# Optimization experiments

Measured on AMD Instinct MI355X. Metric: run time of the kernel, lower is better.

The kernel has to match this reference:

```python
import jax, jax.numpy as jnp
import numpy as np

TOPK = 2


def _conv2d(x, w, b):
    # x: (B, Cin, H, W), w: (Cout, Cin, 3, 3), SAME padding (padding=1)
    y = jax.lax.conv_general_dilated(
        x, w, window_strides=(1, 1), padding='SAME',
        dimension_numbers=('NCHW', 'OIHW', 'NCHW'))
    return y + b[None, :, None, None]


def _msunit(x2d, c1w, c1b, c2w, c2b):
    # TimesNet-style 2D unit: conv(1->d_model) -> GELU -> conv(d_model->1)
    h = jax.nn.gelu(_conv2d(x2d, c1w, c1b))
    return _conv2d(h, c2w, c2b)


def setup_inputs():
    B, T, H, DM = 256, 2048, 720, 64
    key = jax.random.key(0)
    ks = jax.random.split(key, 5)
    x = jax.random.normal(ks[0], (B, 1, T), jnp.float32)
    conv1_w = jax.random.normal(ks[1], (DM, 1, 3, 3), jnp.float32) * 0.1
    conv1_b = jnp.zeros((DM,), jnp.float32)
    conv2_w = jax.random.normal(ks[2], (1, DM, 3, 3), jnp.float32) * 0.1
    conv2_b = jnp.zeros((1,), jnp.float32)
    head_w = jax.random.normal(ks[3], (H, T), jnp.float32) * 0.02
    head_b = jnp.zeros((H,), jnp.float32)
    return {'x': x, 'conv1_w': conv1_w, 'conv1_b': conv1_b,
            'conv2_w': conv2_w, 'conv2_b': conv2_b,
            'head_w': head_w, 'head_b': head_b}


def reference(x, conv1_w, conv1_b, conv2_w, conv2_b, head_w, head_b):
    B, _, T = x.shape
    # FFT amplitude spectrum, batch-averaged, drop DC bin
    amp = jnp.abs(jnp.fft.rfft(x[:, 0, :], axis=-1)).mean(0)[1:]
    vals, idx = jax.lax.top_k(amp, TOPK)
    # data-dependent period selection (mirrors .item() calls in torch -> Python ints)
    freqs = np.asarray(idx) + 1
    P_list = [max(1, int(round(T / int(f)))) for f in freqs]
    weights = jax.nn.softmax(vals.astype(x.dtype))
    y = jnp.zeros_like(x)
    for i, P in enumerate(P_list):
        cols = (T + P - 1) // P
        pad = P * cols - T
        xp = jnp.pad(x, ((0, 0), (0, 0), (0, pad)))
        x2d = xp.reshape(B, 1, cols, P).transpose(0, 1, 3, 2)  # (B,1,P,cols)
        y2d = _msunit(x2d, conv1_w, conv1_b, conv2_w, conv2_b)  # (B,1,P,cols)
        y1d = y2d.transpose(0, 1, 3, 2).reshape(B, 1, cols * P)[..., :T]
        y = y + weights[i] * y1d
    out = y[:, 0, :] @ head_w.T + head_b  # (B, horizon)
    return out
```

## Files before the change

### kernel.cpp

```cpp
#include <hip/hip_runtime.h>
#include <math.h>

#define T_LEN   2048
#define NB      256
#define N_FREQ  1024
#define DMODEL  64
#define HORIZON 720

#define WS_META 0
#define WS_AMP  64
#define WS_Y0   2048
#define WS_Y1   (2048 + NB * T_LEN)

#define PMAX_FAST 191
#define CHUNK   1024
#define NCHUNK  2
#define HSTRIDE 1412
#define ZSLOT   1408
#define XSMAX   1824
#define ZXS     (XSMAX - 1)

typedef _Float16 h4 __attribute__((ext_vector_type(4)));
typedef float    fx4 __attribute__((ext_vector_type(4)));

__device__ __forceinline__ float gelu_fast(float a) {
    float a2 = a * a;
    float z  = a * fmaf(-0.07135481627159498f, a2, -1.5957691216057308f);
    float e  = __expf(z);
    return a * __builtin_amdgcn_rcpf(1.0f + e);
}

__device__ __forceinline__ float2 cmul(float2 a, float2 b) {
    return make_float2(a.x * b.x - a.y * b.y, a.x * b.y + a.y * b.x);
}

__device__ __forceinline__ void compute_meta(const float* __restrict__ amp,
                                             float* sf, int* si, int tid,
                                             int& P1, int& cols1, int& P2, int& cols2,
                                             float& wg1, float& wg2) {
    float* v1s = sf;        float* v2s = sf + 256;
    int*   i1s = si;        int*   i2s = si + 256;
    float4 v4 = ((const float4*)amp)[tid];
    float vv[4] = {v4.x, v4.y, v4.z, v4.w};
    float v1 = -1e30f, v2 = -1e30f; int i1 = 1 << 30, i2 = 1 << 30;
    #pragma unroll
    for (int u = 0; u < 4; ++u) {
        int j = tid * 4 + u;
        float v = vv[u];
        if (v > v1) { v2 = v1; i2 = i1; v1 = v; i1 = j; }
        else if (v > v2) { v2 = v; i2 = j; }
    }
    v1s[tid] = v1; i1s[tid] = i1; v2s[tid] = v2; i2s[tid] = i2;
    __syncthreads();
    for (int st = 128; st > 0; st >>= 1) {
        if (tid < st) {
            float w1 = v1s[tid + st]; int j1 = i1s[tid + st];
            float w2 = v2s[tid + st]; int j2 = i2s[tid + st];
            float a1 = v1s[tid];      int a1i = i1s[tid];
            float a2 = v2s[tid];      int a2i = i2s[tid];
            float n1, n2; int n1i, n2i;
            bool w1_first = (w1 > a1) || (w1 == a1 && j1 < a1i);
            if (w1_first) {
                n1 = w1; n1i = j1;
                bool a1_next = (a1 > w2) || (a1 == w2 && a1i < j2);
                if (a1_next) { n2 = a1; n2i = a1i; } else { n2 = w2; n2i = j2; }
            } else {
                n1 = a1; n1i = a1i;
                bool w1_next = (w1 > a2) || (w1 == a2 && j1 < a2i);
                if (w1_next) { n2 = w1; n2i = j1; } else { n2 = a2; n2i = a2i; }
            }
            v1s[tid] = n1; i1s[tid] = n1i; v2s[tid] = n2; i2s[tid] = n2i;
        }
        __syncthreads();
    }
    float v1f = v1s[0], v2f = v2s[0];
    int f1 = i1s[0] + 1, f2 = i2s[0] + 1;
    __syncthreads();
    P1 = (int)llround(2048.0 / (double)f1); if (P1 < 1) P1 = 1;
    P2 = (int)llround(2048.0 / (double)f2); if (P2 < 1) P2 = 1;
    cols1 = (T_LEN + P1 - 1) / P1;
    cols2 = (T_LEN + P2 - 1) / P2;
    float mx = fmaxf(v1f, v2f);
    float e1 = __expf(v1f - mx), e2 = __expf(v2f - mx);
    float inv = 1.0f / (e1 + e2);
    wg1 = e1 * inv; wg2 = e2 * inv;
}

__global__ __launch_bounds__(1024) void fft_amp_kernel(const float* __restrict__ x,
                                                       float* __restrict__ amp) {
    __shared__ float2 buf0[2048];
    __shared__ float2 buf1[2048];
    __shared__ float2 tw[1024];
    const int tid = threadIdx.x;
    const int b = blockIdx.x;

    {
        float s, c;
        __sincosf((float)tid * 3.0679615757712823e-3f, &s, &c);
        tw[tid] = make_float2(c, -s);
    }
    const float* xa = x + (2 * b) * T_LEN;
    const float* xb = x + (2 * b + 1) * T_LEN;
    buf0[tid]        = make_float2(xa[tid],        xb[tid]);
    buf0[tid + 1024] = make_float2(xa[tid + 1024], xb[tid + 1024]);
    __syncthreads();

    float2* src = buf0;
    float2* dst = buf1;
    for (int s = 0; s < 10; s += 2) {
        const int Ns = 1 << s;
        if (tid < 512) {
            const int j1 = tid;
            const int q  = j1 & (Ns - 1);
            const int hi = j1 >> s;
            float2 A = src[j1];
            float2 B = src[j1 + 1024];
            float2 C = src[j1 + 512];
            float2 D = src[j1 + 1536];
            float2 w  = tw[q << (10 - s)];
            float2 wB = cmul(w, B);
            float2 wD = cmul(w, D);
            float2 P0 = make_float2(A.x + wB.x, A.y + wB.y);
            float2 P1 = make_float2(A.x - wB.x, A.y - wB.y);
            float2 Q0 = make_float2(C.x + wD.x, C.y + wD.y);
            float2 Q1 = make_float2(C.x - wD.x, C.y - wD.y);
            float2 wa = tw[q << (9 - s)];
            float2 wb = tw[(q + Ns) << (9 - s)];
            float2 t0 = cmul(wa, Q0);
            float2 t1 = cmul(wb, Q1);
            const int O = (hi << (s + 2)) + q;
            dst[O]          = make_float2(P0.x + t0.x, P0.y + t0.y);
            dst[O + 2 * Ns] = make_float2(P0.x - t0.x, P0.y - t0.y);
            dst[O + Ns]     = make_float2(P1.x + t1.x, P1.y + t1.y);
            dst[O + 3 * Ns] = make_float2(P1.x - t1.x, P1.y - t1.y);
        }
        __syncthreads();
        float2* tmp = src; src = dst; dst = tmp;
    }
    {
        float2 a  = src[tid];
        float2 bb = src[tid + 1024];
        float2 w  = tw[tid];
        float2 t  = cmul(w, bb);
        dst[tid]        = make_float2(a.x + t.x, a.y + t.y);
        dst[tid + 1024] = make_float2(a.x - t.x, a.y - t.y);
        __syncthreads();
        float2* tmp = src; src = dst; dst = tmp;
    }
    const int kk = (tid + b * 8) & 1023;
    const int k = kk + 1;
    float2 Zk = src[k];
    float2 Zn = src[2048 - k];
    float ar = 0.5f * (Zk.x + Zn.x), ai = 0.5f * (Zk.y - Zn.y);
    float br = 0.5f * (Zk.y + Zn.y), bi = 0.5f * (Zk.x - Zn.x);
    float mag = (sqrtf(ar * ar + ai * ai) + sqrtf(br * br + bi * bi)) * (1.0f / 256.0f);
    atomicAdd(amp + kk, mag);
}

__global__ __launch_bounds__(256) void conv_fast_kernel(
    const float* __restrict__ x,
    const float* __restrict__ w1, const float* __restrict__ b1,
    const float* __restrict__ w2, const float* __restrict__ b2,
    const float* __restrict__ amp,
    float* __restrict__ ws, float* __restrict__ out)
{
    __shared__ float xs[XSMAX];
    __shared__ _Float16 dk[9][HSTRIDE];

    const int tid = threadIdx.x;
    {
        const int bid = blockIdx.y * gridDim.x + blockIdx.x;
        if (tid < 45) {
            int idx = bid * 45 + tid;
            if (idx < (NB * HORIZON) / 4)
                ((float4*)out)[idx] = make_float4(0.f, 0.f, 0.f, 0.f);
        }
    }

    int P1, cols1, P2, cols2; float wg1, wg2;
    compute_meta(amp, xs, (int*)(xs + 512), tid, P1, cols1, P2, cols2, wg1, wg2);

    if (blockIdx.x == 0 && blockIdx.y == 0 && tid == 0) {
        int* mi = (int*)ws;
        mi[0] = P1; mi[1] = cols1; mi[2] = P2; mi[3] = cols2;
        ws[4] = wg1; ws[5] = wg2;
    }

    const int per  = blockIdx.y;
    const int P    = per == 0 ? P1 : P2;
    const int cols = per == 0 ? cols1 : cols2;
    if (P > PMAX_FAST) return;
    const float wgt = per == 0 ? wg1 : wg2;
    float* yout = ws + (per == 0 ? WS_Y0 : WS_Y1);

    const int b   = blockIdx.x >> 1;
    const int ci  = blockIdx.x & 1;
    const int t0  = ci * CHUNK;
    const int U0  = t0 - (P + 1);
    const int HN  = CHUNK + 2 * P + 2;
    const int X0  = t0 - (2 * P + 2);
    const int XN  = CHUNK + 4 * P + 4;

    __syncthreads();
    for (int j = tid; j < XSMAX; j += 256) {
        int t = X0 + j;
        xs[j] = (j < XN && t >= 0 && t < T_LEN) ? x[b * T_LEN + t] : 0.f;
    }
    __syncthreads();

    const int lane = tid & 63;
    const int wv   = tid >> 6;
    const int lm   = lane & 15;
    const int lg   = lane >> 4;

    h4  w1f[4], w2f[4];
    fx4 b1f[4];
    #pragma unroll
    for (int t = 0; t < 4; ++t) {
        #pragma unroll
        for (int i = 0; i < 4; ++i) {
            const int k = lg * 4 + i;
            w1f[t][i] = (_Float16)((k < 9) ? w1[(t * 16 + lm) * 9 + k] : 0.f);
            w2f[t][i] = (_Float16)((lm < 9) ? w2[(t * 16 + k) * 9 + lm] : 0.f);
            b1f[t][i] = b1[t * 16 + k];
        }
    }

    const int HN16 = (HN + 15) >> 4;
    const fx4 zf4 = {0.f, 0.f, 0.f, 0.f};

    for (int nt = wv; nt < HN16; nt += 4) {
        const int ih = nt * 16 + lm;
        const int u  = U0 + ih;
        const int uu = u < 0 ? 0 : u;
        const int cc = uu / P;
        const int pp = uu - cc * P;
        const bool rm = pp > 0, rp = pp < P - 1, cm = cc > 0, cp = (cc + 1) < cols;
        const int ibase = ih + P + 1;
        h4 xb;
        #pragma unroll
        for (int j = 0; j < 4; ++j) {
            const int tap = lg * 4 + j;
            const int q = (tap * 86) >> 8;
            const int r = tap - q * 3;
            const bool ok = (tap < 9)
                && (q > 0 || rm) && (q < 2 || rp)
                && (r > 0 || cm) && (r < 2 || cp);
            const int addr = ok ? (ibase + (r - 1) * P + (q - 1)) : ZXS;
            xb[j] = (_Float16)xs[addr];
        }
        fx4 h0 = __builtin_amdgcn_mfma_f32_16x16x16f16(w1f[0], xb, b1f[0], 0, 0, 0);
        fx4 h1 = __builtin_amdgcn_mfma_f32_16x16x16f16(w1f[1], xb, b1f[1], 0, 0, 0);
        fx4 h2 = __builtin_amdgcn_mfma_f32_16x16x16f16(w1f[2], xb, b1f[2], 0, 0, 0);
        fx4 h3 = __builtin_amdgcn_mfma_f32_16x16x16f16(w1f[3], xb, b1f[3], 0, 0, 0);
        h4 g0, g1, g2, g3;
        #pragma unroll
        for (int i = 0; i < 4; ++i) {
            g0[i] = (_Float16)gelu_fast(h0[i]);
            g1[i] = (_Float16)gelu_fast(h1[i]);
            g2[i] = (_Float16)gelu_fast(h2[i]);
            g3[i] = (_Float16)gelu_fast(h3[i]);
        }
        fx4 da = __builtin_amdgcn_mfma_f32_16x16x16f16(w2f[0], g0, zf4, 0, 0, 0);
        fx4 db = __builtin_amdgcn_mfma_f32_16x16x16f16(w2f[1], g1, zf4, 0, 0, 0);
        da = __builtin_amdgcn_mfma_f32_16x16x16f16(w2f[2], g2, da, 0, 0, 0);
        db = __builtin_amdgcn_mfma_f32_16x16x16f16(w2f[3], g3, db, 0, 0, 0);
        if (ih < HN) {
            #pragma unroll
            for (int i = 0; i < 4; ++i) {
                const int row = lg * 4 + i;
                if (row < 9) dk[row][ih] = (_Float16)(da[i] + db[i]);
            }
        }
    }
    if (tid < 9) dk[tid][ZSLOT] = (_Float16)0.f;
    __syncthreads();

    const float bias2 = b2[0];
    #pragma unroll
    for (int o = 0; o < 4; ++o) {
        const int t = t0 + tid + o * 256;
        const int iout = tid + o * 256 + (P + 1);
        const int cc = t / P;
        const int pp = t - cc * P;
        const bool rm = pp > 0, rp = pp < P - 1, cm = cc > 0, cp = (cc + 1) < cols;
        const int i0 = (rm && cm) ? iout - P - 1 : ZSLOT;
        const int i1 = rm         ? iout - 1     : ZSLOT;
        const int i2 = (rm && cp) ? iout + P - 1 : ZSLOT;
        const int i3 = cm         ? iout - P     : ZSLOT;
        const int i5 = cp         ? iout + P     : ZSLOT;
        const int i6 = (rp && cm) ? iout - P + 1 : ZSLOT;
        const int i7 = rp         ? iout + 1     : ZSLOT;
        const int i8 = (rp && cp) ? iout + P + 1 : ZSLOT;
        float s = (float)dk[4][iout];
        s += (float)dk[0][i0]; s += (float)dk[1][i1]; s += (float)dk[2][i2];
        s += (float)dk[3][i3]; s += (float)dk[5][i5]; s += (float)dk[6][i6];
        s += (float)dk[7][i7]; s += (float)dk[8][i8];
        yout[b * T_LEN + t] = wgt * (s + bias2);
    }
}

__global__ __launch_bounds__(256) void conv_unit_kernel(
    const float* __restrict__ x,
    const float* __restrict__ w1, const float* __restrict__ b1,
    const float* __restrict__ w2, const float* __restrict__ b2,
    float* __restrict__ ws)
{
    const int* mi = (const int*)ws;
    const int per   = blockIdx.y;
    const int P     = mi[per * 2 + 0];
    const int cols  = mi[per * 2 + 1];
    if (P <= PMAX_FAST) return;
    const float wgt = ws[4 + per];
    float* yout = ws + (per == 0 ? WS_Y0 : WS_Y1);

    __shared__ float w1s[DMODEL * 9];
    __shared__ float w2s[DMODEL * 9];
    __shared__ float b1s[DMODEL];
    __shared__ float xs[12][13];
    __shared__ float hs[DMODEL][101];

    const int tid = threadIdx.x;
    for (int i = tid; i < DMODEL * 9; i += 256) { w1s[i] = w1[i]; w2s[i] = w2[i]; }
    if (tid < DMODEL) b1s[tid] = b1[tid];
    const float bias2 = b2[0];

    const int tp = (P + 7) >> 3;
    const int tc = (cols + 7) >> 3;
    const int tiles_img = tp * tc;
    const int total = tiles_img * NB;

    for (int tile = blockIdx.x; tile < total; tile += gridDim.x) {
        const int b   = tile / tiles_img;
        const int ti  = tile - b * tiles_img;
        const int tpi = ti / tc;
        const int tci = ti - tpi * tc;
        const int p0 = tpi * 8, c0 = tci * 8;

        __syncthreads();
        if (tid < 144) {
            int i = tid / 12, j = tid - (tid / 12) * 12;
            int pp = p0 - 2 + i, cc = c0 - 2 + j;
            float v = 0.f;
            if (pp >= 0 && pp < P && cc >= 0 && cc < cols) {
                int t = cc * P + pp;
                if (t < T_LEN) v = x[b * T_LEN + t];
            }
            xs[i][j] = v;
        }
        __syncthreads();

        #pragma unroll
        for (int it = 0; it < 25; ++it) {
            int idx = it * 256 + tid;
            int ch = idx / 100;
            int px = idx - ch * 100;
            int pi = px / 10;
            int pj = px - pi * 10;
            const float* w = &w1s[ch * 9];
            float a = b1s[ch];
            a = fmaf(w[0], xs[pi    ][pj    ], a);
            a = fmaf(w[1], xs[pi    ][pj + 1], a);
            a = fmaf(w[2], xs[pi    ][pj + 2], a);
            a = fmaf(w[3], xs[pi + 1][pj    ], a);
            a = fmaf(w[4], xs[pi + 1][pj + 1], a);
            a = fmaf(w[5], xs[pi + 1][pj + 2], a);
            a = fmaf(w[6], xs[pi + 2][pj    ], a);
            a = fmaf(w[7], xs[pi + 2][pj + 1], a);
            a = fmaf(w[8], xs[pi + 2][pj + 2], a);
            float g = gelu_fast(a);
            int pp = p0 - 1 + pi, cc = c0 - 1 + pj;
            bool in_img = (pp >= 0) & (pp < P) & (cc >= 0) & (cc < cols);
            hs[ch][px] = in_img ? g : 0.0f;
        }
        __syncthreads();

        {
            const int pixel = tid >> 2, part = tid & 3;
            const int pi = pixel >> 3, pj = pixel & 7;
            const int base = pi * 10 + pj;
            float s = 0.f;
            for (int ch = part * 16; ch < part * 16 + 16; ++ch) {
                const float* w  = &w2s[ch * 9];
                const float* hr = &hs[ch][base];
                s = fmaf(w[0], hr[0],  s);
                s = fmaf(w[1], hr[1],  s);
                s = fmaf(w[2], hr[2],  s);
                s = fmaf(w[3], hr[10], s);
                s = fmaf(w[4], hr[11], s);
                s = fmaf(w[5], hr[12], s);
                s = fmaf(w[6], hr[20], s);
                s = fmaf(w[7], hr[21], s);
                s = fmaf(w[8], hr[22], s);
            }
            s += __shfl_down(s, 1);
            s += __shfl_down(s, 2);
            if (part == 0) {
                int pp = p0 + pi, cc = c0 + pj;
                if (pp < P && cc < cols) {
                    int t = cc * P + pp;
                    if (t < T_LEN) yout[b * T_LEN + t] = wgt * (s + bias2);
                }
            }
        }
    }
}

__global__ __launch_bounds__(256) void head_gemm_kernel(
    const float* __restrict__ ws, const float* __restrict__ hw,
    const float* __restrict__ hb, float* __restrict__ out)
{
    const float* y0 = ws + WS_Y0;
    const float* y1 = ws + WS_Y1;
    const int b0 = blockIdx.x * 32, h0 = blockIdx.y * 32;
    const int kc0 = blockIdx.z * 512;
    __shared__ float As[32][33];
    __shared__ float Bs[32][33];
    const int tid = threadIdx.x;
    const int tx = tid & 15, ty = tid >> 4;
    const int i0 = ty * 2, j0 = tx * 2;
    const int sr = tid >> 3;
    const int sc = (tid & 7) * 4;
    float a00 = 0.f, a01 = 0.f, a10 = 0.f, a11 = 0.f;
    for (int k0 = kc0; k0 < kc0 + 512; k0 += 32) {
        {
            const int src = (b0 + sr) * T_LEN + k0 + sc;
            float4 u = *(const float4*)(y0 + src);
            float4 v = *(const float4*)(y1 + src);
            As[sr][sc]     = u.x + v.x;
            As[sr][sc + 1] = u.y + v.y;
            As[sr][sc + 2] = u.z + v.z;
            As[sr][sc + 3] = u.w + v.w;
            const int hrow = h0 + sr;
            float4 w = (hrow < HORIZON) ? *(const float4*)(hw + hrow * T_LEN + k0 + sc)
                                        : make_float4(0.f, 0.f, 0.f, 0.f);
            Bs[sr][sc]     = w.x;
            Bs[sr][sc + 1] = w.y;
            Bs[sr][sc + 2] = w.z;
            Bs[sr][sc + 3] = w.w;
        }
        __syncthreads();
        #pragma unroll
        for (int kk = 0; kk < 32; ++kk) {
            float av0 = As[i0][kk], av1 = As[i0 + 1][kk];
            float bv0 = Bs[j0][kk], bv1 = Bs[j0 + 1][kk];
            a00 = fmaf(av0, bv0, a00); a01 = fmaf(av0, bv1, a01);
            a10 = fmaf(av1, bv0, a10); a11 = fmaf(av1, bv1, a11);
        }
        __syncthreads();
    }
    const int bi = b0 + i0, hj = h0 + j0;
    if (blockIdx.z == 0) {
        if (hj < HORIZON)     { float bb = hb[hj];     a00 += bb; a10 += bb; }
        if (hj + 1 < HORIZON) { float bb = hb[hj + 1]; a01 += bb; a11 += bb; }
    }
    if (hj < HORIZON) {
        atomicAdd(&out[bi * HORIZON + hj], a00);
        atomicAdd(&out[(bi + 1) * HORIZON + hj], a10);
    }
    if (hj + 1 < HORIZON) {
        atomicAdd(&out[bi * HORIZON + hj + 1], a01);
        atomicAdd(&out[(bi + 1) * HORIZON + hj + 1], a11);
    }
}

extern "C" void kernel_launch(void* const* d_in, const int* in_sizes, int n_in,
                              void* d_out, int out_size, void* d_ws, size_t ws_size,
                              hipStream_t stream) {
    const float* x   = (const float*)d_in[0];
    const float* c1w = (const float*)d_in[1];
    const float* c1b = (const float*)d_in[2];
    const float* c2w = (const float*)d_in[3];
    const float* c2b = (const float*)d_in[4];
    const float* hw  = (const float*)d_in[5];
    const float* hb  = (const float*)d_in[6];
    float* out = (float*)d_out;
    float* ws  = (float*)d_ws;

    float* amp = ws + WS_AMP;

    hipMemsetAsync(amp, 0, N_FREQ * sizeof(float), stream);
    fft_amp_kernel<<<NB / 2, 1024, 0, stream>>>(x, amp);
    conv_fast_kernel<<<dim3(NB * NCHUNK, 2), 256, 0, stream>>>(x, c1w, c1b, c2w, c2b, amp, ws, out);
    conv_unit_kernel<<<dim3(256, 2), 256, 0, stream>>>(x, c1w, c1b, c2w, c2b, ws);
    head_gemm_kernel<<<dim3(NB / 32, (HORIZON + 31) / 32, 4), 256, 0, stream>>>(ws, hw, hb, out);
}
```

Measured before the change: 152.6 us.

## Use half-length real FFT, smaller conv chunks, and magic-number division

The FFT kernel now computes each real row's spectrum with a 1024-point complex FFT of packed even/odd samples plus a twiddle post-pass, using one 256-thread block per row instead of two rows per 1024-thread block. The conv kernel halves its time chunk to 512 and doubles the block count, which shrinks shared memory per block and may raise occupancy, at the cost of more halo recomputation. Integer division by the period is replaced with a multiply-high by a precomputed reciprocal. The P<2 case is routed to the generic kernel so the magic division stays valid.

```diff
diff --git a/kernel.cpp b/kernel.cpp
--- a/kernel.cpp
+++ b/kernel.cpp
@@ -13,11 +13,11 @@
 #define WS_Y1   (2048 + NB * T_LEN)
 
 #define PMAX_FAST 191
-#define CHUNK   1024
-#define NCHUNK  2
-#define HSTRIDE 1412
-#define ZSLOT   1408
-#define XSMAX   1824
+#define CHUNK   512
+#define NCHUNK  4
+#define HSTRIDE 904
+#define ZSLOT   898
+#define XSMAX   1312
 #define ZXS     (XSMAX - 1)
 
 typedef _Float16 h4 __attribute__((ext_vector_type(4)));
@@ -32,6 +32,10 @@
 
 __device__ __forceinline__ float2 cmul(float2 a, float2 b) {
     return make_float2(a.x * b.x - a.y * b.y, a.x * b.y + a.y * b.x);
+}
+
+__device__ __forceinline__ unsigned magic_div(unsigned d) {
+    return (unsigned)((0x100000000ULL + d - 1) / d);
 }
 
 __device__ __forceinline__ void compute_meta(const float* __restrict__ amp,
@@ -86,75 +90,80 @@
     wg1 = e1 * inv; wg2 = e2 * inv;
 }
 
-__global__ __launch_bounds__(1024) void fft_amp_kernel(const float* __restrict__ x,
-                                                       float* __restrict__ amp) {
-    __shared__ float2 buf0[2048];
-    __shared__ float2 buf1[2048];
-    __shared__ float2 tw[1024];
+__global__ __launch_bounds__(256) void fft_amp_kernel(const float* __restrict__ x,
+                                                      float* __restrict__ amp) {
+    __shared__ float2 buf0[1024];
+    __shared__ float2 buf1[1024];
+    __shared__ float2 tw[512];
     const int tid = threadIdx.x;
     const int b = blockIdx.x;
 
     {
         float s, c;
-        __sincosf((float)tid * 3.0679615757712823e-3f, &s, &c);
+        __sincosf((float)tid * 6.135923151542565e-3f, &s, &c);
         tw[tid] = make_float2(c, -s);
-    }
-    const float* xa = x + (2 * b) * T_LEN;
-    const float* xb = x + (2 * b + 1) * T_LEN;
-    buf0[tid]        = make_float2(xa[tid],        xb[tid]);
-    buf0[tid + 1024] = make_float2(xa[tid + 1024], xb[tid + 1024]);
+        __sincosf((float)(tid + 256) * 6.135923151542565e-3f, &s, &c);
+        tw[tid + 256] = make_float2(c, -s);
+    }
+    const float2* xz = (const float2*)(x + b * T_LEN);
+    buf0[tid]       = xz[tid];
+    buf0[tid + 256] = xz[tid + 256];
+    buf0[tid + 512] = xz[tid + 512];
+    buf0[tid + 768] = xz[tid + 768];
     __syncthreads();
 
     float2* src = buf0;
     float2* dst = buf1;
     for (int s = 0; s < 10; s += 2) {
         const int Ns = 1 << s;
-        if (tid < 512) {
-            const int j1 = tid;
-            const int q  = j1 & (Ns - 1);
-            const int hi = j1 >> s;
-            float2 A = src[j1];
-            float2 B = src[j1 + 1024];
-            float2 C = src[j1 + 512];
-            float2 D = src[j1 + 1536];
-            float2 w  = tw[q << (10 - s)];
-            float2 wB = cmul(w, B);
-            float2 wD = cmul(w, D);
-            float2 P0 = make_float2(A.x + wB.x, A.y + wB.y);
-            float2 P1 = make_float2(A.x - wB.x, A.y - wB.y);
-            float2 Q0 = make_float2(C.x + wD.x, C.y + wD.y);
-            float2 Q1 = make_float2(C.x - wD.x, C.y - wD.y);
-            float2 wa = tw[q << (9 - s)];
-            float2 wb = tw[(q + Ns) << (9 - s)];
-            float2 t0 = cmul(wa, Q0);
-            float2 t1 = cmul(wb, Q1);
-            const int O = (hi << (s + 2)) + q;
-            dst[O]          = make_float2(P0.x + t0.x, P0.y + t0.y);
-            dst[O + 2 * Ns] = make_float2(P0.x - t0.x, P0.y - t0.y);
-            dst[O + Ns]     = make_float2(P1.x + t1.x, P1.y + t1.y);
-            dst[O + 3 * Ns] = make_float2(P1.x - t1.x, P1.y - t1.y);
-        }
+        const int j1 = tid;
+        const int q  = j1 & (Ns - 1);
+        const int hi = j1 >> s;
+        float2 A = src[j1];
+        float2 B = src[j1 + 512];
+        float2 C = src[j1 + 256];
+        float2 D = src[j1 + 768];
+        float2 w  = tw[q << (9 - s)];
+        float2 wB = cmul(w, B);
+        float2 wD = cmul(w, D);
+        float2 P0 = make_float2(A.x + wB.x, A.y + wB.y);
+        float2 P1 = make_float2(A.x - wB.x, A.y - wB.y);
+        float2 Q0 = make_float2(C.x + wD.x, C.y + wD.y);
+        float2 Q1 = make_float2(C.x - wD.x, C.y - wD.y);
+        float2 wa = tw[q << (8 - s)];
+        float2 wb = tw[(q + Ns) << (8 - s)];
+        float2 t0 = cmul(wa, Q0);
+        float2 t1 = cmul(wb, Q1);
+        const int O = (hi << (s + 2)) + q;
+        dst[O]          = make_float2(P0.x + t0.x, P0.y + t0.y);
+        dst[O + 2 * Ns] = make_float2(P0.x - t0.x, P0.y - t0.y);
+        dst[O + Ns]     = make_float2(P1.x + t1.x, P1.y + t1.y);
+        dst[O + 3 * Ns] = make_float2(P1.x - t1.x, P1.y - t1.y);
         __syncthreads();
         float2* tmp = src; src = dst; dst = tmp;
     }
-    {
-        float2 a  = src[tid];
-        float2 bb = src[tid + 1024];
-        float2 w  = tw[tid];
-        float2 t  = cmul(w, bb);
-        dst[tid]        = make_float2(a.x + t.x, a.y + t.y);
-        dst[tid + 1024] = make_float2(a.x - t.x, a.y - t.y);
-        __syncthreads();
-        float2* tmp = src; src = dst; dst = tmp;
-    }
-    const int kk = (tid + b * 8) & 1023;
-    const int k = kk + 1;
-    float2 Zk = src[k];
-    float2 Zn = src[2048 - k];
-    float ar = 0.5f * (Zk.x + Zn.x), ai = 0.5f * (Zk.y - Zn.y);
-    float br = 0.5f * (Zk.y + Zn.y), bi = 0.5f * (Zk.x - Zn.x);
-    float mag = (sqrtf(ar * ar + ai * ai) + sqrtf(br * br + bi * bi)) * (1.0f / 256.0f);
-    atomicAdd(amp + kk, mag);
+    const int rot = (b * 8) & 1023;
+    #pragma unroll
+    for (int j = 0; j < 4; ++j) {
+        const int kk = (tid + j * 256 + rot) & 1023;
+        const int k  = kk + 1;
+        float mag;
+        if (k == 1024) {
+            float2 Z0 = src[0];
+            mag = fabsf(Z0.x - Z0.y) * (1.0f / 256.0f);
+        } else {
+            float2 Zk = src[k];
+            float2 Zn = src[1024 - k];
+            float Ax = 0.5f * (Zk.x + Zn.x), Ay = 0.5f * (Zk.y - Zn.y);
+            float Bx = 0.5f * (Zk.y + Zn.y), By = -0.5f * (Zk.x - Zn.x);
+            float sn, cs;
+            __sincosf((float)k * 3.0679615757712823e-3f, &sn, &cs);
+            float Xx = Ax + cs * Bx + sn * By;
+            float Xy = Ay + cs * By - sn * Bx;
+            mag = sqrtf(Xx * Xx + Xy * Xy) * (1.0f / 256.0f);
+        }
+        atomicAdd(amp + kk, mag);
+    }
 }
 
 __global__ __launch_bounds__(256) void conv_fast_kernel(
@@ -170,8 +179,8 @@
     const int tid = threadIdx.x;
     {
         const int bid = blockIdx.y * gridDim.x + blockIdx.x;
-        if (tid < 45) {
-            int idx = bid * 45 + tid;
+        if (tid < 23) {
+            int idx = bid * 23 + tid;
             if (idx < (NB * HORIZON) / 4)
                 ((float4*)out)[idx] = make_float4(0.f, 0.f, 0.f, 0.f);
         }
@@ -189,22 +198,24 @@
     const int per  = blockIdx.y;
     const int P    = per == 0 ? P1 : P2;
     const int cols = per == 0 ? cols1 : cols2;
-    if (P > PMAX_FAST) return;
+    if (P > PMAX_FAST || P < 2) return;
     const float wgt = per == 0 ? wg1 : wg2;
     float* yout = ws + (per == 0 ? WS_Y0 : WS_Y1);
 
-    const int b   = blockIdx.x >> 1;
-    const int ci  = blockIdx.x & 1;
+    const int b   = blockIdx.x >> 2;
+    const int ci  = blockIdx.x & 3;
     const int t0  = ci * CHUNK;
     const int U0  = t0 - (P + 1);
     const int HN  = CHUNK + 2 * P + 2;
     const int X0  = t0 - (2 * P + 2);
     const int XN  = CHUNK + 4 * P + 4;
-
-    __syncthreads();
+    const unsigned MP = magic_div((unsigned)P);
+
+    __syncthreads();
+    const int bT = b * T_LEN;
     for (int j = tid; j < XSMAX; j += 256) {
         int t = X0 + j;
-        xs[j] = (j < XN && t >= 0 && t < T_LEN) ? x[b * T_LEN + t] : 0.f;
+        xs[j] = (j < XN && t >= 0 && t < T_LEN) ? x[bT + t] : 0.f;
     }
     __syncthreads();
 
@@ -233,7 +244,7 @@
         const int ih = nt * 16 + lm;
         const int u  = U0 + ih;
         const int uu = u < 0 ? 0 : u;
-        const int cc = uu / P;
+        const int cc = (int)__umulhi((unsigned)uu, MP);
         const int pp = uu - cc * P;
         const bool rm = pp > 0, rp = pp < P - 1, cm = cc > 0, cp = (cc + 1) < cols;
         const int ibase = ih + P + 1;
@@ -278,10 +289,10 @@
 
     const float bias2 = b2[0];
     #pragma unroll
-    for (int o = 0; o < 4; ++o) {
+    for (int o = 0; o < 2; ++o) {
         const int t = t0 + tid + o * 256;
         const int iout = tid + o * 256 + (P + 1);
-        const int cc = t / P;
+        const int cc = (int)__umulhi((unsigned)t, MP);
         const int pp = t - cc * P;
         const bool rm = pp > 0, rp = pp < P - 1, cm = cc > 0, cp = (cc + 1) < cols;
         const int i0 = (rm && cm) ? iout - P - 1 : ZSLOT;
@@ -296,7 +307,7 @@
         s += (float)dk[0][i0]; s += (float)dk[1][i1]; s += (float)dk[2][i2];
         s += (float)dk[3][i3]; s += (float)dk[5][i5]; s += (float)dk[6][i6];
         s += (float)dk[7][i7]; s += (float)dk[8][i8];
-        yout[b * T_LEN + t] = wgt * (s + bias2);
+        yout[bT + t] = wgt * (s + bias2);
     }
 }
 
@@ -310,7 +321,7 @@
     const int per   = blockIdx.y;
     const int P     = mi[per * 2 + 0];
     const int cols  = mi[per * 2 + 1];
-    if (P <= PMAX_FAST) return;
+    if (P <= PMAX_FAST && P >= 2) return;
     const float wgt = ws[4 + per];
     float* yout = ws + (per == 0 ? WS_Y0 : WS_Y1);
 
@@ -480,7 +491,7 @@
     float* amp = ws + WS_AMP;
 
     hipMemsetAsync(amp, 0, N_FREQ * sizeof(float), stream);
-    fft_amp_kernel<<<NB / 2, 1024, 0, stream>>>(x, amp);
+    fft_amp_kernel<<<NB, 256, 0, stream>>>(x, amp);
     conv_fast_kernel<<<dim3(NB * NCHUNK, 2), 256, 0, stream>>>(x, c1w, c1b, c2w, c2b, amp, ws, out);
     conv_unit_kernel<<<dim3(256, 2), 256, 0, stream>>>(x, c1w, c1b, c2w, c2b, ws);
     head_gemm_kernel<<<dim3(NB / 32, (HORIZON + 31) / 32, 4), 256, 0, stream>>>(ws, hw, hb, out);
```

Result: slower. 157.5 us (+3.3%).
